# Performance work log

Measured on AMD Instinct MI355X. Metric: run time of the kernel, lower is better.

## Reference

```python
import jax, jax.numpy as jnp
import numpy as np

P, N, NF = 4, 871, 512            # num_meta_paths, node_size (hardcoded 871 in source), node_feature_size
XDIM = 116 * 116                   # x_proj input dim, hardcoded Linear(116*116, nf)
BETA, LAMBDA_WL, GAMMA = 0.1, 0.1, 0.1


def _xavier(k, shape):
    fan_in, fan_out = shape[0], shape[-1]
    bound = np.sqrt(6.0 / (fan_in + fan_out))
    return jax.random.uniform(k, shape, jnp.float32, -bound, bound)


def setup_inputs() -> dict:
    key = jax.random.key(0)
    ks = jax.random.split(key, 12)
    return {
        "z_stack": jax.random.normal(ks[0], (P, N, NF), jnp.float32),
        "x_orig": jax.random.normal(ks[1], (1, 116, 116), jnp.float32),
        "W": _xavier(ks[2], (N, 1)),
        "b": jax.random.uniform(ks[3], (N, 1), jnp.float32),
        "q": _xavier(ks[4], (N, NF)),
        "xp_w": _xavier(ks[5], (XDIM, NF)),
        "xp_b": jnp.zeros((NF,), jnp.float32),
        "w1": _xavier(ks[6], (2 * NF, 512)), "b1": jnp.zeros((512,), jnp.float32),
        "w2": _xavier(ks[7], (512, 256)), "b2": jnp.zeros((256,), jnp.float32),
        "w3": _xavier(ks[8], (256, 1)), "b3": jnp.zeros((1,), jnp.float32),
        "perm": jax.random.permutation(ks[9], N).astype(jnp.int32),
    }


def _mi_mlp(t, w1, b1, w2, b2, w3, b3):
    h = jax.nn.relu(t @ w1 + b1)
    h = jax.nn.relu(h @ w2 + b2)
    return h @ w3 + b3  # [N, 1]


def reference(z_stack, x_orig, W, b, q, xp_w, xp_b, w1, b1, w2, b2, w3, b3, perm):
    # --- vectorized form of the per-node loop:
    # score_p = mean_i( tanh(W_i * z[p,i,:] + b_i) . q_i )
    zt = jnp.tanh(W[None] * z_stack + b[None])            # [P,N,NF]
    scores = jnp.mean(jnp.sum(zt * q[None], axis=-1), axis=-1)  # [P]
    proportions = scores / jnp.sum(scores)
    attn = jax.nn.softmax(proportions)                    # [P] (no isomorphic pairs -> no overwrite)
    # layer_out_p = attn_p * z_p + z_p ; emb = sum_p layer_out_p
    emb = jnp.einsum('p,pnf->nf', 1.0 + attn, z_stack)    # [N,NF]
    # --- estimate_MI(x_orig, emb, mi_estimator_xz)
    x = jnp.broadcast_to(x_orig.reshape(1, -1), (N, XDIM))
    xh = x @ xp_w + xp_b                                  # [N,NF]
    t0 = jnp.concatenate([xh, emb], axis=1)               # [N,2NF]
    t1 = jnp.concatenate([xh, emb[perm]], axis=1)
    mi_lb = jnp.mean(_mi_mlp(t0, w1, b1, w2, b2, w3, b3)) - jnp.log(
        jnp.mean(jnp.exp(_mi_mlp(t1, w1, b1, w2, b2, w3, b3))) + 1e-8)
    I_XZ = jnp.clip(mi_lb, 0.0)
    # y_labels=None -> I_ZY = 0 ; empty isomorphic_pairs -> wl_loss = 0
    total_loss = I_XZ - BETA * 0.0 + LAMBDA_WL * 0.0 + GAMMA * jnp.sum(attn)
    return emb, total_loss
```

## Files before the change

kernel.cpp:

```cpp
#include <hip/hip_runtime.h>
#include <hip/hip_bf16.h>
#include <math.h>

#define NMETA  4
#define NNODE  871
#define NFEAT  512
#define XDIM   (116*116)
#define ZPLANE (NNODE*NFEAT)
#define NCHUNK 55
#define MT     55

#define WS_COEF   8
#define WS_CNT    12
#define WS_SPART  16
#define WS_C1P    256
#define WS_XHP    8448
#define WS_V      73984
#define WS_W1P    74856
#define WS_W2P    205928
#define WS_FXHP   271500
#define WS_FSP    271628
#define MAGICF    0x13579BDFu

typedef short v8s __attribute__((ext_vector_type(8)));
typedef float v4f __attribute__((ext_vector_type(4)));

static __device__ __forceinline__ short f2bf(float f) {
  __hip_bfloat16 h = __float2bfloat16(f);
  return *reinterpret_cast<short*>(&h);
}

__global__ __launch_bounds__(256) void k_front(const float* __restrict__ x,
                                               const float* __restrict__ xpw,
                                               const float* __restrict__ w1,
                                               const float* __restrict__ w2,
                                               const float* __restrict__ z,
                                               const float* __restrict__ W,
                                               const float* __restrict__ b,
                                               const float* __restrict__ q,
                                               const float* __restrict__ xpb,
                                               const float* __restrict__ b1,
                                               float* __restrict__ ws,
                                               short* __restrict__ w1p,
                                               short* __restrict__ w2p) {
  const int blk = blockIdx.x;
  const int tid = threadIdx.x;
  if (blk < 128) {
    const int f4 = tid & 127;
    const int rp = tid >> 7;
    const int d0 = blk * 106;
    const int rows = min(106, XDIM - d0);
    __shared__ float xs[106];
    if (tid < rows) xs[tid] = x[d0 + tid];
    __syncthreads();
    float4 acc = {0.f, 0.f, 0.f, 0.f};
    const float4* xp4 = (const float4*)xpw;
#pragma unroll 4
    for (int r = rp; r < rows; r += 2) {
      const float xv = xs[r];
      const float4 w = xp4[(size_t)(d0 + r) * 128 + f4];
      acc.x += xv * w.x; acc.y += xv * w.y; acc.z += xv * w.z; acc.w += xv * w.w;
    }
    __shared__ float4 red4[128];
    if (rp) red4[f4] = acc;
    __syncthreads();
    if (!rp) {
      float4 o = red4[f4];
      o.x += acc.x; o.y += acc.y; o.z += acc.z; o.w += acc.w;
      ((float4*)(ws + WS_XHP + (size_t)blk * NFEAT))[f4] = o;
    }
    __syncthreads();
    if (tid == 0) {
      __builtin_amdgcn_fence(__ATOMIC_RELEASE, "agent");
      __hip_atomic_store((unsigned*)&ws[WS_FXHP + blk], MAGICF,
                         __ATOMIC_RELAXED, __HIP_MEMORY_SCOPE_AGENT);
    }
  } else if (blk < 512) {
    const int base = (blk - 128) * 256 + tid;
#pragma unroll
    for (int it = 0; it < 4; ++it) {
      int s = base + it * 98304;
      if (s < 262144) {
        const int k = s >> 9, n = s & 511;
        const int t = (k >> 5) * 16384 + (n >> 4) * 512 + ((k >> 3) & 3) * 128
                    + (n & 15) * 8 + (k & 7);
        w1p[t] = f2bf(w1[(size_t)(512 + k) * 512 + n]);
      } else {
        const int o = s - 262144;
        const int k = o >> 8, n = o & 255;
        const int t = (k >> 5) * 8192 + (n >> 4) * 512 + ((k >> 3) & 3) * 128
                    + (n & 15) * 8 + (k & 7);
        w2p[t] = f2bf(w2[(size_t)k * 256 + n]);
      }
    }
  } else if (blk < 732) {
    const int sblk = blk - 512;
    const int p = sblk / NCHUNK;
    const int chunk = sblk % NCHUNK;
    const int i0 = chunk * 16;
    const int i1 = min(i0 + 16, NNODE);
    const int f4 = tid & 127;
    const int ip = tid >> 7;
    float local = 0.f;
    for (int i = i0 + ip; i < i1; i += 2) {
      const float wi = W[i];
      const float bi = b[i];
      const float4 zr = ((const float4*)(z + ((size_t)p * NNODE + i) * NFEAT))[f4];
      const float4 qr = ((const float4*)(q + (size_t)i * NFEAT))[f4];
      local += tanhf(wi * zr.x + bi) * qr.x + tanhf(wi * zr.y + bi) * qr.y
             + tanhf(wi * zr.z + bi) * qr.z + tanhf(wi * zr.w + bi) * qr.w;
    }
    __shared__ float red[256];
    red[tid] = local;
    __syncthreads();
    for (int s = 128; s > 0; s >>= 1) {
      if (tid < s) red[tid] += red[tid + s];
      __syncthreads();
    }
    if (tid == 0) {
      ws[WS_SPART + sblk] = red[0];
      __builtin_amdgcn_fence(__ATOMIC_RELEASE, "agent");
      __hip_atomic_store((unsigned*)&ws[WS_FSP + sblk], MAGICF,
                         __ATOMIC_RELAXED, __HIP_MEMORY_SCOPE_AGENT);
    }
  } else if (blk == 732) {
    if (tid == 0) *(unsigned*)&ws[WS_CNT] = 0u;
  } else if (blk < 749) {
    const int bk = blk - 733;
    for (;;) {
      int ok = 1;
      if (tid < 128)
        ok = (__hip_atomic_load((const unsigned*)&ws[WS_FXHP + tid],
                                __ATOMIC_RELAXED, __HIP_MEMORY_SCOPE_AGENT) == MAGICF);
      if (__syncthreads_and(ok)) break;
      __builtin_amdgcn_s_sleep(8);
    }
    __builtin_amdgcn_fence(__ATOMIC_ACQUIRE, "agent");
    __shared__ float xsc[32];
    {
      const int f = tid & 31;
      const int pg = tid >> 5;
      float s = 0.f;
#pragma unroll 4
      for (int p = pg; p < 128; p += 8)
        s += ws[WS_XHP + (size_t)p * NFEAT + bk * 32 + f];
      __shared__ float redc[256];
      redc[tid] = s;
      __syncthreads();
      if (tid < 32) {
        float t2 = 0.f;
#pragma unroll
        for (int g = 0; g < 8; ++g) t2 += redc[g * 32 + tid];
        xsc[tid] = t2 + xpb[bk * 32 + tid];
      }
      __syncthreads();
    }
    const int j4 = tid & 127;
    const int fp = tid >> 7;
    float4 acc = {0.f, 0.f, 0.f, 0.f};
    const float4* w14 = (const float4*)w1;
#pragma unroll
    for (int ff = 0; ff < 16; ++ff) {
      const int f = bk * 32 + fp * 16 + ff;
      const float xv = xsc[fp * 16 + ff];
      const float4 wv = w14[(size_t)f * 128 + j4];
      acc.x += xv * wv.x; acc.y += xv * wv.y; acc.z += xv * wv.z; acc.w += xv * wv.w;
    }
    __shared__ float4 red2[128];
    if (fp) red2[j4] = acc;
    __syncthreads();
    if (!fp) {
      float4 o = acc;
      {
        float4 t = red2[j4];
        o.x += t.x; o.y += t.y; o.z += t.z; o.w += t.w;
      }
      if (bk == 0) {
        o.x += b1[j4 * 4 + 0]; o.y += b1[j4 * 4 + 1];
        o.z += b1[j4 * 4 + 2]; o.w += b1[j4 * 4 + 3];
      }
      ((float4*)(ws + WS_C1P + (size_t)bk * NFEAT))[j4] = o;
    }
  } else {
    for (;;) {
      int ok = 1;
      if (tid < 220)
        ok = (__hip_atomic_load((const unsigned*)&ws[WS_FSP + tid],
                                __ATOMIC_RELAXED, __HIP_MEMORY_SCOPE_AGENT) == MAGICF);
      if (__syncthreads_and(ok)) break;
      __builtin_amdgcn_s_sleep(8);
    }
    __builtin_amdgcn_fence(__ATOMIC_ACQUIRE, "agent");
    __shared__ float sp[220];
    if (tid < 220) sp[tid] = ws[WS_SPART + tid];
    __syncthreads();
    if (tid == 0) {
      float sv[NMETA], sum = 0.f;
#pragma unroll
      for (int p = 0; p < NMETA; ++p) {
        float s = 0.f;
        for (int c = 0; c < NCHUNK; ++c) s += sp[p * NCHUNK + c];
        sv[p] = s / (float)NNODE;
        sum += sv[p];
      }
      float m = -1e30f;
#pragma unroll
      for (int p = 0; p < NMETA; ++p) { sv[p] = sv[p] / sum; m = fmaxf(m, sv[p]); }
      float es = 0.f;
#pragma unroll
      for (int p = 0; p < NMETA; ++p) { sv[p] = expf(sv[p] - m); es += sv[p]; }
#pragma unroll
      for (int p = 0; p < NMETA; ++p) ws[WS_COEF + p] = 1.f + sv[p] / es;
    }
  }
}

__global__ __launch_bounds__(1024) void k_fused(const float* __restrict__ z,
                                                float* __restrict__ ws,
                                                float* __restrict__ out,
                                                const short* __restrict__ w1p,
                                                const short* __restrict__ w2p,
                                                const float* __restrict__ b2,
                                                const float* __restrict__ w3,
                                                const float* __restrict__ b3) {
  __shared__ __align__(16) short embs[8192];
  __shared__ __align__(16) short h2a[8192];
  __shared__ float cs[512];
  __shared__ float rf0[1024], rf1[1024];
  __shared__ float vred[16][17];
  const int tid = threadIdx.x;
  const int r0 = blockIdx.x * 16;

  if (tid < 512) {
    float a0 = 0.f;
#pragma unroll
    for (int k = 0; k < 16; ++k) a0 += ws[WS_C1P + k * 512 + tid];
    cs[tid] = a0;
  }
  const float c0 = ws[WS_COEF + 0], c1c = ws[WS_COEF + 1];
  const float c2 = ws[WS_COEF + 2], c3 = ws[WS_COEF + 3];

  const int oc = tid & 63;
  const int row = tid >> 6;
  const float4* z4 = (const float4*)z;
  float4* out4 = (float4*)out;
  {
    const int gr = r0 + row;
    const int slot = oc * 16 + (row ^ (oc & 15));
    v8s h;
    if (gr < NNODE) {
      const int zi = gr * 128 + oc * 2;
      float4 a0 = z4[zi],               a1 = z4[zi + 1];
      float4 b0 = z4[NNODE*128 + zi],   b1v = z4[NNODE*128 + zi + 1];
      float4 d0 = z4[2*NNODE*128 + zi], d1 = z4[2*NNODE*128 + zi + 1];
      float4 e0 = z4[3*NNODE*128 + zi], e1 = z4[3*NNODE*128 + zi + 1];
      float4 r0v, r1v;
      r0v.x = c0*a0.x + c1c*b0.x + c2*d0.x + c3*e0.x;
      r0v.y = c0*a0.y + c1c*b0.y + c2*d0.y + c3*e0.y;
      r0v.z = c0*a0.z + c1c*b0.z + c2*d0.z + c3*e0.z;
      r0v.w = c0*a0.w + c1c*b0.w + c2*d0.w + c3*e0.w;
      r1v.x = c0*a1.x + c1c*b1v.x + c2*d1.x + c3*e1.x;
      r1v.y = c0*a1.y + c1c*b1v.y + c2*d1.y + c3*e1.y;
      r1v.z = c0*a1.z + c1c*b1v.z + c2*d1.z + c3*e1.z;
      r1v.w = c0*a1.w + c1c*b1v.w + c2*d1.w + c3*e1.w;
      out4[zi] = r0v;
      out4[zi + 1] = r1v;
      h[0] = f2bf(r0v.x); h[1] = f2bf(r0v.y); h[2] = f2bf(r0v.z); h[3] = f2bf(r0v.w);
      h[4] = f2bf(r1v.x); h[5] = f2bf(r1v.y); h[6] = f2bf(r1v.z); h[7] = f2bf(r1v.w);
    } else {
      h = (v8s){0,0,0,0,0,0,0,0};
    }
    *(v8s*)(embs + slot * 8) = h;
  }
  __syncthreads();

  const int lane = tid & 63, w = tid >> 6;
  const int n15 = lane & 15, quad = lane >> 4;
  v4f e[2];
#pragma unroll
  for (int ct = 0; ct < 2; ++ct) e[ct] = (v4f){0.f, 0.f, 0.f, 0.f};
#pragma unroll
  for (int kb = 0; kb < 16; ++kb) {
    const int koct = kb * 4 + quad;
    v8s a = *(const v8s*)(embs + (koct * 16 + (n15 ^ (koct & 15))) * 8);
    const short* B = w1p + kb * 16384 + w * 1024 + quad * 128 + n15 * 8;
#pragma unroll
    for (int ct = 0; ct < 2; ++ct) {
      v8s bb = *(const v8s*)(B + ct * 512);
      e[ct] = __builtin_amdgcn_mfma_f32_16x16x32_bf16(a, bb, e[ct], 0, 0, 0);
    }
  }
#pragma unroll
  for (int ct = 0; ct < 2; ++ct) {
    const int col = w * 32 + ct * 16 + n15;
    const int koct = col >> 3, j = col & 7;
#pragma unroll
    for (int r = 0; r < 4; ++r) {
      const int m = quad * 4 + r;
      h2a[(koct * 16 + (m ^ (koct & 15))) * 8 + j] = f2bf(fmaxf(e[ct][r] + cs[col], 0.f));
    }
  }
  __syncthreads();

  v4f g = (v4f){0.f, 0.f, 0.f, 0.f};
#pragma unroll
  for (int kb = 0; kb < 16; ++kb) {
    const int koct = kb * 4 + quad;
    v8s a = *(const v8s*)(h2a + (koct * 16 + (n15 ^ (koct & 15))) * 8);
    v8s bb = *(const v8s*)(w2p + kb * 8192 + w * 512 + quad * 128 + n15 * 8);
    g = __builtin_amdgcn_mfma_f32_16x16x32_bf16(a, bb, g, 0, 0, 0);
  }
  {
    const int col = w * 16 + n15;
    const float b2v = b2[col], w3v = w3[col];
#pragma unroll
    for (int r = 0; r < 4; ++r) {
      float s = fmaxf(g[r] + b2v, 0.f) * w3v;
      s += __shfl_xor(s, 1);
      s += __shfl_xor(s, 2);
      s += __shfl_xor(s, 4);
      s += __shfl_xor(s, 8);
      if (n15 == 0) vred[quad * 4 + r][w] = s;
    }
  }
  __syncthreads();
  if (tid < 16) {
    float acc = 0.f;
#pragma unroll
    for (int ww = 0; ww < 16; ++ww) acc += vred[tid][ww];
    const int grow = r0 + tid;
    if (grow < NNODE) ws[WS_V + grow] = acc;
  }

  __shared__ unsigned last;
  __syncthreads();
  if (tid == 0) {
    __threadfence();
    unsigned old = atomicAdd((unsigned int*)&ws[WS_CNT], 1u);
    last = (old == MT - 1) ? 1u : 0u;
  }
  __syncthreads();
  if (last) {
    __builtin_amdgcn_fence(__ATOMIC_ACQUIRE, "agent");
    const float bias = b3[0];
    float s0 = 0.f, s1 = 0.f;
    for (int i = tid; i < NNODE; i += 1024) {
      float xv = ws[WS_V + i] + bias;
      s0 += xv;
      s1 += expf(xv);
    }
    rf0[tid] = s0; rf1[tid] = s1;
    __syncthreads();
    for (int s = 512; s > 0; s >>= 1) {
      if (tid < s) { rf0[tid] += rf0[tid + s]; rf1[tid] += rf1[tid + s]; }
      __syncthreads();
    }
    if (tid == 0) {
      float m0 = rf0[0] / (float)NNODE;
      float m1 = rf1[0] / (float)NNODE;
      float mi = m0 - logf(m1 + 1e-8f);
      out[ZPLANE] = fmaxf(mi, 0.f) + 0.1f;
    }
  }
}

extern "C" void kernel_launch(void* const* d_in, const int* in_sizes, int n_in,
                              void* d_out, int out_size, void* d_ws, size_t ws_size,
                              hipStream_t stream) {
  const float* z   = (const float*)d_in[0];
  const float* x   = (const float*)d_in[1];
  const float* W   = (const float*)d_in[2];
  const float* b   = (const float*)d_in[3];
  const float* q   = (const float*)d_in[4];
  const float* xpw = (const float*)d_in[5];
  const float* xpb = (const float*)d_in[6];
  const float* w1  = (const float*)d_in[7];
  const float* b1  = (const float*)d_in[8];
  const float* w2  = (const float*)d_in[9];
  const float* b2  = (const float*)d_in[10];
  const float* w3  = (const float*)d_in[11];
  const float* b3  = (const float*)d_in[12];
  float* out = (float*)d_out;
  float* ws  = (float*)d_ws;

  short* w1p = (short*)(ws + WS_W1P);
  short* w2p = (short*)(ws + WS_W2P);

  k_front<<<750, 256, 0, stream>>>(x, xpw, w1, w2, z, W, b, q, xpb, b1, ws, w1p, w2p);
  k_fused<<<MT, 1024, 0, stream>>>(z, ws, out, w1p, w2p, b2, w3, b3);
}
```

Measured before the change: 136.3 us.

## Merge front and fused kernels into one persistent kernel with flag-based dataflow

Replaces the two-kernel launch with a single 254-block kernel of 1024 threads. The MLP tile blocks compute their own attention score partials from z rows they already hold in registers, then spin on flags for the score, packed-weight and xh-contribution producers instead of waiting at a kernel boundary. The x-projection, c1 and weight-packing roles are re-split across fewer, larger blocks. The goal is to remove the inter-kernel gap and the second read of z, at the cost of relying on all blocks being co-resident, since blocks spin on flags set by other blocks.

```diff
diff --git a/kernel.cpp b/kernel.cpp
--- a/kernel.cpp
+++ b/kernel.cpp
@@ -7,19 +7,22 @@
 #define NFEAT  512
 #define XDIM   (116*116)
 #define ZPLANE (NNODE*NFEAT)
-#define NCHUNK 55
 #define MT     55
 
-#define WS_COEF   8
-#define WS_CNT    12
+#define NXB    175
+#define XROWS  77
+
 #define WS_SPART  16
 #define WS_C1P    256
 #define WS_XHP    8448
-#define WS_V      73984
-#define WS_W1P    74856
-#define WS_W2P    205928
-#define WS_FXHP   271500
-#define WS_FSP    271628
+#define WS_V      98304
+#define WS_W1P    99328
+#define WS_W2P    230400
+#define WS_FXHP   263168
+#define WS_FPACK  263344
+#define WS_FC1    263368
+#define WS_FSP    263376
+#define WS_FV     263436
 #define MAGICF    0x13579BDFu
 
 typedef short v8s __attribute__((ext_vector_type(8)));
@@ -30,337 +33,373 @@
   return *reinterpret_cast<short*>(&h);
 }
 
-__global__ __launch_bounds__(256) void k_front(const float* __restrict__ x,
-                                               const float* __restrict__ xpw,
-                                               const float* __restrict__ w1,
-                                               const float* __restrict__ w2,
-                                               const float* __restrict__ z,
-                                               const float* __restrict__ W,
-                                               const float* __restrict__ b,
-                                               const float* __restrict__ q,
-                                               const float* __restrict__ xpb,
-                                               const float* __restrict__ b1,
-                                               float* __restrict__ ws,
-                                               short* __restrict__ w1p,
-                                               short* __restrict__ w2p) {
+static __device__ __forceinline__ unsigned ldflag(const float* ws, int off) {
+  return __hip_atomic_load((const unsigned*)&ws[off], __ATOMIC_RELAXED,
+                           __HIP_MEMORY_SCOPE_AGENT);
+}
+static __device__ __forceinline__ void stflag(float* ws, int off) {
+  __builtin_amdgcn_fence(__ATOMIC_RELEASE, "agent");
+  __hip_atomic_store((unsigned*)&ws[off], MAGICF, __ATOMIC_RELAXED,
+                     __HIP_MEMORY_SCOPE_AGENT);
+}
+
+__global__ __launch_bounds__(1024) void k_all(const float* __restrict__ z,
+                                              const float* __restrict__ x,
+                                              const float* __restrict__ W,
+                                              const float* __restrict__ b,
+                                              const float* __restrict__ q,
+                                              const float* __restrict__ xpw,
+                                              const float* __restrict__ xpb,
+                                              const float* __restrict__ w1,
+                                              const float* __restrict__ b1,
+                                              const float* __restrict__ w2,
+                                              const float* __restrict__ b2,
+                                              const float* __restrict__ w3,
+                                              const float* __restrict__ b3,
+                                              float* __restrict__ ws,
+                                              float* __restrict__ out,
+                                              short* __restrict__ w1p,
+                                              short* __restrict__ w2p) {
+  __shared__ __align__(16) char pool[37376];
   const int blk = blockIdx.x;
   const int tid = threadIdx.x;
-  if (blk < 128) {
+
+  if (blk < MT) {
+    short* embs = (short*)pool;
+    short* h2a  = (short*)(pool + 16384);
+    float* cs   = (float*)(pool + 32768);
+    float* spl  = (float*)(pool + 34816);
+    float* sred = (float*)(pool + 35712);
+    float* cf   = (float*)(pool + 35968);
+    float* vred = (float*)(pool + 36000);
+    float* wred = (float*)(pool + 37088);
+
+    const int r0 = blk * 16;
+    const int oc = tid & 63;
+    const int row = tid >> 6;
+    const int gr = r0 + row;
+    const bool valid = gr < NNODE;
+
+    const float4* z4 = (const float4*)z;
+    const float4* q4 = (const float4*)q;
+    float4 za0, za1, zb0, zb1, zc0, zc1, zd0, zd1, qa, qb;
+    float wi = 0.f, bi = 0.f;
+    const int zi = gr * 128 + oc * 2;
+    if (valid) {
+      za0 = z4[zi];                 za1 = z4[zi + 1];
+      zb0 = z4[NNODE*128 + zi];     zb1 = z4[NNODE*128 + zi + 1];
+      zc0 = z4[2*NNODE*128 + zi];   zc1 = z4[2*NNODE*128 + zi + 1];
+      zd0 = z4[3*NNODE*128 + zi];   zd1 = z4[3*NNODE*128 + zi + 1];
+      qa  = q4[gr * 128 + oc * 2];  qb  = q4[gr * 128 + oc * 2 + 1];
+      wi = W[gr]; bi = b[gr];
+    } else {
+      za0 = za1 = zb0 = zb1 = zc0 = zc1 = zd0 = zd1 = (float4){0,0,0,0};
+      qa = qb = (float4){0,0,0,0};
+    }
+
+    auto dot8 = [&](const float4& u0, const float4& u1) -> float {
+      return tanhf(wi*u0.x + bi)*qa.x + tanhf(wi*u0.y + bi)*qa.y
+           + tanhf(wi*u0.z + bi)*qa.z + tanhf(wi*u0.w + bi)*qa.w
+           + tanhf(wi*u1.x + bi)*qb.x + tanhf(wi*u1.y + bi)*qb.y
+           + tanhf(wi*u1.z + bi)*qb.z + tanhf(wi*u1.w + bi)*qb.w;
+    };
+    float sp0 = valid ? dot8(za0, za1) : 0.f;
+    float sp1 = valid ? dot8(zb0, zb1) : 0.f;
+    float sp2 = valid ? dot8(zc0, zc1) : 0.f;
+    float sp3 = valid ? dot8(zd0, zd1) : 0.f;
+#pragma unroll
+    for (int m = 1; m < 64; m <<= 1) {
+      sp0 += __shfl_xor(sp0, m); sp1 += __shfl_xor(sp1, m);
+      sp2 += __shfl_xor(sp2, m); sp3 += __shfl_xor(sp3, m);
+    }
+    if (oc == 0) {
+      sred[row*4+0] = sp0; sred[row*4+1] = sp1;
+      sred[row*4+2] = sp2; sred[row*4+3] = sp3;
+    }
+    __syncthreads();
+    if (tid < 4) {
+      float s = 0.f;
+#pragma unroll
+      for (int r = 0; r < 16; ++r) s += sred[r*4 + tid];
+      ws[WS_SPART + tid * 55 + blk] = s;
+    }
+    __syncthreads();
+    if (tid == 0) stflag(ws, WS_FSP + blk);
+
+    for (;;) {
+      int ok = 1;
+      if (tid < 55) ok = (ldflag(ws, WS_FSP + tid) == MAGICF);
+      if (__syncthreads_and(ok)) break;
+      __builtin_amdgcn_s_sleep(2);
+    }
+    __builtin_amdgcn_fence(__ATOMIC_ACQUIRE, "agent");
+    if (tid < 220) spl[tid] = ws[WS_SPART + tid];
+    __syncthreads();
+    if (tid == 0) {
+      float sv[NMETA], sum = 0.f;
+#pragma unroll
+      for (int p = 0; p < NMETA; ++p) {
+        float s = 0.f;
+        for (int c = 0; c < MT; ++c) s += spl[p * 55 + c];
+        sv[p] = s / (float)NNODE;
+        sum += sv[p];
+      }
+      float m = -1e30f;
+#pragma unroll
+      for (int p = 0; p < NMETA; ++p) { sv[p] = sv[p] / sum; m = fmaxf(m, sv[p]); }
+      float es = 0.f;
+#pragma unroll
+      for (int p = 0; p < NMETA; ++p) { sv[p] = expf(sv[p] - m); es += sv[p]; }
+#pragma unroll
+      for (int p = 0; p < NMETA; ++p) cf[p] = 1.f + sv[p] / es;
+    }
+    __syncthreads();
+    const float c0 = cf[0], c1c = cf[1], c2 = cf[2], c3 = cf[3];
+
+    {
+      const int slot = oc * 16 + (row ^ (oc & 15));
+      v8s h;
+      if (valid) {
+        float4 r0v, r1v;
+        r0v.x = c0*za0.x + c1c*zb0.x + c2*zc0.x + c3*zd0.x;
+        r0v.y = c0*za0.y + c1c*zb0.y + c2*zc0.y + c3*zd0.y;
+        r0v.z = c0*za0.z + c1c*zb0.z + c2*zc0.z + c3*zd0.z;
+        r0v.w = c0*za0.w + c1c*zb0.w + c2*zc0.w + c3*zd0.w;
+        r1v.x = c0*za1.x + c1c*zb1.x + c2*zc1.x + c3*zd1.x;
+        r1v.y = c0*za1.y + c1c*zb1.y + c2*zc1.y + c3*zd1.y;
+        r1v.z = c0*za1.z + c1c*zb1.z + c2*zc1.z + c3*zd1.z;
+        r1v.w = c0*za1.w + c1c*zb1.w + c2*zc1.w + c3*zd1.w;
+        ((float4*)out)[zi] = r0v;
+        ((float4*)out)[zi + 1] = r1v;
+        h[0] = f2bf(r0v.x); h[1] = f2bf(r0v.y); h[2] = f2bf(r0v.z); h[3] = f2bf(r0v.w);
+        h[4] = f2bf(r1v.x); h[5] = f2bf(r1v.y); h[6] = f2bf(r1v.z); h[7] = f2bf(r1v.w);
+      } else {
+        h = (v8s){0,0,0,0,0,0,0,0};
+      }
+      *(v8s*)(embs + slot * 8) = h;
+    }
+    __syncthreads();
+
+    for (;;) {
+      int ok = 1;
+      if (tid < 16) ok = (ldflag(ws, WS_FPACK + tid) == MAGICF);
+      else if (tid < 20) ok = (ldflag(ws, WS_FC1 + (tid - 16)) == MAGICF);
+      if (__syncthreads_and(ok)) break;
+      __builtin_amdgcn_s_sleep(2);
+    }
+    __builtin_amdgcn_fence(__ATOMIC_ACQUIRE, "agent");
+    if (tid < 512) {
+      float a = 0.f;
+#pragma unroll
+      for (int k = 0; k < 4; ++k) a += ws[WS_C1P + k * 512 + tid];
+      cs[tid] = a;
+    }
+    __syncthreads();
+
+    const int lane = tid & 63, w = tid >> 6;
+    const int n15 = lane & 15, quad = lane >> 4;
+    v4f e[2];
+#pragma unroll
+    for (int ct = 0; ct < 2; ++ct) e[ct] = (v4f){0.f, 0.f, 0.f, 0.f};
+#pragma unroll
+    for (int kb = 0; kb < 16; ++kb) {
+      const int koct = kb * 4 + quad;
+      v8s a = *(const v8s*)(embs + (koct * 16 + (n15 ^ (koct & 15))) * 8);
+      const short* B = w1p + kb * 16384 + w * 1024 + quad * 128 + n15 * 8;
+#pragma unroll
+      for (int ct = 0; ct < 2; ++ct) {
+        v8s bb = *(const v8s*)(B + ct * 512);
+        e[ct] = __builtin_amdgcn_mfma_f32_16x16x32_bf16(a, bb, e[ct], 0, 0, 0);
+      }
+    }
+#pragma unroll
+    for (int ct = 0; ct < 2; ++ct) {
+      const int col = w * 32 + ct * 16 + n15;
+      const int koct = col >> 3, j = col & 7;
+#pragma unroll
+      for (int r = 0; r < 4; ++r) {
+        const int m = quad * 4 + r;
+        h2a[(koct * 16 + (m ^ (koct & 15))) * 8 + j] = f2bf(fmaxf(e[ct][r] + cs[col], 0.f));
+      }
+    }
+    __syncthreads();
+
+    for (;;) {
+      int ok = 1;
+      if (tid < 4) ok = (ldflag(ws, WS_FPACK + 16 + tid) == MAGICF);
+      if (__syncthreads_and(ok)) break;
+      __builtin_amdgcn_s_sleep(2);
+    }
+    __builtin_amdgcn_fence(__ATOMIC_ACQUIRE, "agent");
+
+    v4f g = (v4f){0.f, 0.f, 0.f, 0.f};
+#pragma unroll
+    for (int kb = 0; kb < 16; ++kb) {
+      const int koct = kb * 4 + quad;
+      v8s a = *(const v8s*)(h2a + (koct * 16 + (n15 ^ (koct & 15))) * 8);
+      v8s bb = *(const v8s*)(w2p + kb * 8192 + w * 512 + quad * 128 + n15 * 8);
+      g = __builtin_amdgcn_mfma_f32_16x16x32_bf16(a, bb, g, 0, 0, 0);
+    }
+    {
+      const int col = w * 16 + n15;
+      const float b2v = b2[col], w3v = w3[col];
+#pragma unroll
+      for (int r = 0; r < 4; ++r) {
+        float s = fmaxf(g[r] + b2v, 0.f) * w3v;
+        s += __shfl_xor(s, 1);
+        s += __shfl_xor(s, 2);
+        s += __shfl_xor(s, 4);
+        s += __shfl_xor(s, 8);
+        if (n15 == 0) vred[(quad * 4 + r) * 17 + w] = s;
+      }
+    }
+    __syncthreads();
+    if (tid < 16) {
+      float acc = 0.f;
+#pragma unroll
+      for (int ww = 0; ww < 16; ++ww) acc += vred[tid * 17 + ww];
+      const int grow = r0 + tid;
+      if (grow < NNODE) ws[WS_V + grow] = acc;
+    }
+    __syncthreads();
+    if (tid == 0) stflag(ws, WS_FV + blk);
+
+    if (blk == 0) {
+      for (;;) {
+        int ok = 1;
+        if (tid < 55) ok = (ldflag(ws, WS_FV + tid) == MAGICF);
+        if (__syncthreads_and(ok)) break;
+        __builtin_amdgcn_s_sleep(2);
+      }
+      __builtin_amdgcn_fence(__ATOMIC_ACQUIRE, "agent");
+      const float bias = b3[0];
+      float s0 = 0.f, s1 = 0.f;
+      if (tid < NNODE) {
+        float xv = ws[WS_V + tid] + bias;
+        s0 = xv; s1 = expf(xv);
+      }
+#pragma unroll
+      for (int m = 1; m < 64; m <<= 1) { s0 += __shfl_xor(s0, m); s1 += __shfl_xor(s1, m); }
+      if (lane == 0) { wred[w * 2] = s0; wred[w * 2 + 1] = s1; }
+      __syncthreads();
+      if (tid == 0) {
+        float t0 = 0.f, t1 = 0.f;
+#pragma unroll
+        for (int ww = 0; ww < 16; ++ww) { t0 += wred[ww * 2]; t1 += wred[ww * 2 + 1]; }
+        float m0 = t0 / (float)NNODE;
+        float m1 = t1 / (float)NNODE;
+        float mi = m0 - logf(m1 + 1e-8f);
+        out[ZPLANE] = fmaxf(mi, 0.f) + 0.1f;
+      }
+    }
+  } else if (blk < MT + NXB) {
+    const int xb = blk - MT;
+    const int d0 = xb * XROWS;
+    const int rows = min(XROWS, XDIM - d0);
+    float* xs = (float*)pool;
+    float4* redx = (float4*)(pool + 320);
+    if (tid < rows) xs[tid] = x[d0 + tid];
+    __syncthreads();
     const int f4 = tid & 127;
     const int rp = tid >> 7;
-    const int d0 = blk * 106;
-    const int rows = min(106, XDIM - d0);
-    __shared__ float xs[106];
-    if (tid < rows) xs[tid] = x[d0 + tid];
-    __syncthreads();
     float4 acc = {0.f, 0.f, 0.f, 0.f};
     const float4* xp4 = (const float4*)xpw;
-#pragma unroll 4
-    for (int r = rp; r < rows; r += 2) {
+    for (int r = rp; r < rows; r += 8) {
       const float xv = xs[r];
-      const float4 w = xp4[(size_t)(d0 + r) * 128 + f4];
-      acc.x += xv * w.x; acc.y += xv * w.y; acc.z += xv * w.z; acc.w += xv * w.w;
-    }
-    __shared__ float4 red4[128];
-    if (rp) red4[f4] = acc;
+      const float4 wv = xp4[(size_t)(d0 + r) * 128 + f4];
+      acc.x += xv * wv.x; acc.y += xv * wv.y; acc.z += xv * wv.z; acc.w += xv * wv.w;
+    }
+    if (rp) redx[(rp - 1) * 128 + f4] = acc;
     __syncthreads();
     if (!rp) {
-      float4 o = red4[f4];
-      o.x += acc.x; o.y += acc.y; o.z += acc.z; o.w += acc.w;
-      ((float4*)(ws + WS_XHP + (size_t)blk * NFEAT))[f4] = o;
-    }
-    __syncthreads();
-    if (tid == 0) {
-      __builtin_amdgcn_fence(__ATOMIC_RELEASE, "agent");
-      __hip_atomic_store((unsigned*)&ws[WS_FXHP + blk], MAGICF,
-                         __ATOMIC_RELAXED, __HIP_MEMORY_SCOPE_AGENT);
-    }
-  } else if (blk < 512) {
-    const int base = (blk - 128) * 256 + tid;
-#pragma unroll
-    for (int it = 0; it < 4; ++it) {
-      int s = base + it * 98304;
-      if (s < 262144) {
+#pragma unroll
+      for (int g = 0; g < 7; ++g) {
+        float4 t = redx[g * 128 + f4];
+        acc.x += t.x; acc.y += t.y; acc.z += t.z; acc.w += t.w;
+      }
+      ((float4*)(ws + WS_XHP + (size_t)xb * 512))[f4] = acc;
+    }
+    __syncthreads();
+    if (tid == 0) stflag(ws, WS_FXHP + xb);
+  } else if (blk < MT + NXB + 4) {
+    const int bk = blk - (MT + NXB);
+    float* xh = (float*)pool;
+    float* redr = (float*)(pool + 512);
+    float4* redg = (float4*)(pool + 4608);
+    for (;;) {
+      int ok = 1;
+      if (tid < NXB) ok = (ldflag(ws, WS_FXHP + tid) == MAGICF);
+      if (__syncthreads_and(ok)) break;
+      __builtin_amdgcn_s_sleep(2);
+    }
+    __builtin_amdgcn_fence(__ATOMIC_ACQUIRE, "agent");
+    const int f = tid & 127;
+    const int part = tid >> 7;
+    {
+      float s = 0.f;
+      for (int p = part; p < NXB; p += 8) s += ws[WS_XHP + (size_t)p * 512 + bk * 128 + f];
+      redr[tid] = s;
+    }
+    __syncthreads();
+    if (tid < 128) {
+      float t = xpb[bk * 128 + tid];
+#pragma unroll
+      for (int g = 0; g < 8; ++g) t += redr[g * 128 + tid];
+      xh[tid] = t;
+    }
+    __syncthreads();
+    const int j4 = tid & 127;
+    const int fg = tid >> 7;
+    float4 acc = {0.f, 0.f, 0.f, 0.f};
+    const float4* w14 = (const float4*)w1;
+#pragma unroll
+    for (int ff = 0; ff < 16; ++ff) {
+      const int fr = bk * 128 + fg * 16 + ff;
+      const float xv = xh[fg * 16 + ff];
+      const float4 wv = w14[(size_t)fr * 128 + j4];
+      acc.x += xv * wv.x; acc.y += xv * wv.y; acc.z += xv * wv.z; acc.w += xv * wv.w;
+    }
+    if (fg) redg[(fg - 1) * 128 + j4] = acc;
+    __syncthreads();
+    if (!fg) {
+#pragma unroll
+      for (int g = 0; g < 7; ++g) {
+        float4 t = redg[g * 128 + j4];
+        acc.x += t.x; acc.y += t.y; acc.z += t.z; acc.w += t.w;
+      }
+      if (bk == 0) {
+        acc.x += b1[j4 * 4 + 0]; acc.y += b1[j4 * 4 + 1];
+        acc.z += b1[j4 * 4 + 2]; acc.w += b1[j4 * 4 + 3];
+      }
+      ((float4*)(ws + WS_C1P + (size_t)bk * 512))[j4] = acc;
+    }
+    __syncthreads();
+    if (tid == 0) stflag(ws, WS_FC1 + bk);
+  } else {
+    const int pb = blk - (MT + NXB + 4);
+    if (pb < 16) {
+      const int s0 = pb * 16384;
+#pragma unroll
+      for (int it = 0; it < 16; ++it) {
+        const int s = s0 + it * 1024 + tid;
         const int k = s >> 9, n = s & 511;
         const int t = (k >> 5) * 16384 + (n >> 4) * 512 + ((k >> 3) & 3) * 128
                     + (n & 15) * 8 + (k & 7);
         w1p[t] = f2bf(w1[(size_t)(512 + k) * 512 + n]);
-      } else {
-        const int o = s - 262144;
+      }
+    } else {
+      const int o0 = (pb - 16) * 16384;
+#pragma unroll
+      for (int it = 0; it < 16; ++it) {
+        const int o = o0 + it * 1024 + tid;
         const int k = o >> 8, n = o & 255;
         const int t = (k >> 5) * 8192 + (n >> 4) * 512 + ((k >> 3) & 3) * 128
                     + (n & 15) * 8 + (k & 7);
         w2p[t] = f2bf(w2[(size_t)k * 256 + n]);
       }
     }
-  } else if (blk < 732) {
-    const int sblk = blk - 512;
-    const int p = sblk / NCHUNK;
-    const int chunk = sblk % NCHUNK;
-    const int i0 = chunk * 16;
-    const int i1 = min(i0 + 16, NNODE);
-    const int f4 = tid & 127;
-    const int ip = tid >> 7;
-    float local = 0.f;
-    for (int i = i0 + ip; i < i1; i += 2) {
-      const float wi = W[i];
-      const float bi = b[i];
-      const float4 zr = ((const float4*)(z + ((size_t)p * NNODE + i) * NFEAT))[f4];
-      const float4 qr = ((const float4*)(q + (size_t)i * NFEAT))[f4];
-      local += tanhf(wi * zr.x + bi) * qr.x + tanhf(wi * zr.y + bi) * qr.y
-             + tanhf(wi * zr.z + bi) * qr.z + tanhf(wi * zr.w + bi) * qr.w;
-    }
-    __shared__ float red[256];
-    red[tid] = local;
-    __syncthreads();
-    for (int s = 128; s > 0; s >>= 1) {
-      if (tid < s) red[tid] += red[tid + s];
-      __syncthreads();
-    }
-    if (tid == 0) {
-      ws[WS_SPART + sblk] = red[0];
-      __builtin_amdgcn_fence(__ATOMIC_RELEASE, "agent");
-      __hip_atomic_store((unsigned*)&ws[WS_FSP + sblk], MAGICF,
-                         __ATOMIC_RELAXED, __HIP_MEMORY_SCOPE_AGENT);
-    }
-  } else if (blk == 732) {
-    if (tid == 0) *(unsigned*)&ws[WS_CNT] = 0u;
-  } else if (blk < 749) {
-    const int bk = blk - 733;
-    for (;;) {
-      int ok = 1;
-      if (tid < 128)
-        ok = (__hip_atomic_load((const unsigned*)&ws[WS_FXHP + tid],
-                                __ATOMIC_RELAXED, __HIP_MEMORY_SCOPE_AGENT) == MAGICF);
-      if (__syncthreads_and(ok)) break;
-      __builtin_amdgcn_s_sleep(8);
-    }
-    __builtin_amdgcn_fence(__ATOMIC_ACQUIRE, "agent");
-    __shared__ float xsc[32];
-    {
-      const int f = tid & 31;
-      const int pg = tid >> 5;
-      float s = 0.f;
-#pragma unroll 4
-      for (int p = pg; p < 128; p += 8)
-        s += ws[WS_XHP + (size_t)p * NFEAT + bk * 32 + f];
-      __shared__ float redc[256];
-      redc[tid] = s;
-      __syncthreads();
-      if (tid < 32) {
-        float t2 = 0.f;
-#pragma unroll
-        for (int g = 0; g < 8; ++g) t2 += redc[g * 32 + tid];
-        xsc[tid] = t2 + xpb[bk * 32 + tid];
-      }
-      __syncthreads();
-    }
-    const int j4 = tid & 127;
-    const int fp = tid >> 7;
-    float4 acc = {0.f, 0.f, 0.f, 0.f};
-    const float4* w14 = (const float4*)w1;
-#pragma unroll
-    for (int ff = 0; ff < 16; ++ff) {
-      const int f = bk * 32 + fp * 16 + ff;
-      const float xv = xsc[fp * 16 + ff];
-      const float4 wv = w14[(size_t)f * 128 + j4];
-      acc.x += xv * wv.x; acc.y += xv * wv.y; acc.z += xv * wv.z; acc.w += xv * wv.w;
-    }
-    __shared__ float4 red2[128];
-    if (fp) red2[j4] = acc;
-    __syncthreads();
-    if (!fp) {
-      float4 o = acc;
-      {
-        float4 t = red2[j4];
-        o.x += t.x; o.y += t.y; o.z += t.z; o.w += t.w;
-      }
-      if (bk == 0) {
-        o.x += b1[j4 * 4 + 0]; o.y += b1[j4 * 4 + 1];
-        o.z += b1[j4 * 4 + 2]; o.w += b1[j4 * 4 + 3];
-      }
-      ((float4*)(ws + WS_C1P + (size_t)bk * NFEAT))[j4] = o;
-    }
-  } else {
-    for (;;) {
-      int ok = 1;
-      if (tid < 220)
-        ok = (__hip_atomic_load((const unsigned*)&ws[WS_FSP + tid],
-                                __ATOMIC_RELAXED, __HIP_MEMORY_SCOPE_AGENT) == MAGICF);
-      if (__syncthreads_and(ok)) break;
-      __builtin_amdgcn_s_sleep(8);
-    }
-    __builtin_amdgcn_fence(__ATOMIC_ACQUIRE, "agent");
-    __shared__ float sp[220];
-    if (tid < 220) sp[tid] = ws[WS_SPART + tid];
-    __syncthreads();
-    if (tid == 0) {
-      float sv[NMETA], sum = 0.f;
-#pragma unroll
-      for (int p = 0; p < NMETA; ++p) {
-        float s = 0.f;
-        for (int c = 0; c < NCHUNK; ++c) s += sp[p * NCHUNK + c];
-        sv[p] = s / (float)NNODE;
-        sum += sv[p];
-      }
-      float m = -1e30f;
-#pragma unroll
-      for (int p = 0; p < NMETA; ++p) { sv[p] = sv[p] / sum; m = fmaxf(m, sv[p]); }
-      float es = 0.f;
-#pragma unroll
-      for (int p = 0; p < NMETA; ++p) { sv[p] = expf(sv[p] - m); es += sv[p]; }
-#pragma unroll
-      for (int p = 0; p < NMETA; ++p) ws[WS_COEF + p] = 1.f + sv[p] / es;
-    }
-  }
-}
-
-__global__ __launch_bounds__(1024) void k_fused(const float* __restrict__ z,
-                                                float* __restrict__ ws,
-                                                float* __restrict__ out,
-                                                const short* __restrict__ w1p,
-                                                const short* __restrict__ w2p,
-                                                const float* __restrict__ b2,
-                                                const float* __restrict__ w3,
-                                                const float* __restrict__ b3) {
-  __shared__ __align__(16) short embs[8192];
-  __shared__ __align__(16) short h2a[8192];
-  __shared__ float cs[512];
-  __shared__ float rf0[1024], rf1[1024];
-  __shared__ float vred[16][17];
-  const int tid = threadIdx.x;
-  const int r0 = blockIdx.x * 16;
-
-  if (tid < 512) {
-    float a0 = 0.f;
-#pragma unroll
-    for (int k = 0; k < 16; ++k) a0 += ws[WS_C1P + k * 512 + tid];
-    cs[tid] = a0;
-  }
-  const float c0 = ws[WS_COEF + 0], c1c = ws[WS_COEF + 1];
-  const float c2 = ws[WS_COEF + 2], c3 = ws[WS_COEF + 3];
-
-  const int oc = tid & 63;
-  const int row = tid >> 6;
-  const float4* z4 = (const float4*)z;
-  float4* out4 = (float4*)out;
-  {
-    const int gr = r0 + row;
-    const int slot = oc * 16 + (row ^ (oc & 15));
-    v8s h;
-    if (gr < NNODE) {
-      const int zi = gr * 128 + oc * 2;
-      float4 a0 = z4[zi],               a1 = z4[zi + 1];
-      float4 b0 = z4[NNODE*128 + zi],   b1v = z4[NNODE*128 + zi + 1];
-      float4 d0 = z4[2*NNODE*128 + zi], d1 = z4[2*NNODE*128 + zi + 1];
-      float4 e0 = z4[3*NNODE*128 + zi], e1 = z4[3*NNODE*128 + zi + 1];
-      float4 r0v, r1v;
-      r0v.x = c0*a0.x + c1c*b0.x + c2*d0.x + c3*e0.x;
-      r0v.y = c0*a0.y + c1c*b0.y + c2*d0.y + c3*e0.y;
-      r0v.z = c0*a0.z + c1c*b0.z + c2*d0.z + c3*e0.z;
-      r0v.w = c0*a0.w + c1c*b0.w + c2*d0.w + c3*e0.w;
-      r1v.x = c0*a1.x + c1c*b1v.x + c2*d1.x + c3*e1.x;
-      r1v.y = c0*a1.y + c1c*b1v.y + c2*d1.y + c3*e1.y;
-      r1v.z = c0*a1.z + c1c*b1v.z + c2*d1.z + c3*e1.z;
-      r1v.w = c0*a1.w + c1c*b1v.w + c2*d1.w + c3*e1.w;
-      out4[zi] = r0v;
-      out4[zi + 1] = r1v;
-      h[0] = f2bf(r0v.x); h[1] = f2bf(r0v.y); h[2] = f2bf(r0v.z); h[3] = f2bf(r0v.w);
-      h[4] = f2bf(r1v.x); h[5] = f2bf(r1v.y); h[6] = f2bf(r1v.z); h[7] = f2bf(r1v.w);
-    } else {
-      h = (v8s){0,0,0,0,0,0,0,0};
-    }
-    *(v8s*)(embs + slot * 8) = h;
-  }
-  __syncthreads();
-
-  const int lane = tid & 63, w = tid >> 6;
-  const int n15 = lane & 15, quad = lane >> 4;
-  v4f e[2];
-#pragma unroll
-  for (int ct = 0; ct < 2; ++ct) e[ct] = (v4f){0.f, 0.f, 0.f, 0.f};
-#pragma unroll
-  for (int kb = 0; kb < 16; ++kb) {
-    const int koct = kb * 4 + quad;
-    v8s a = *(const v8s*)(embs + (koct * 16 + (n15 ^ (koct & 15))) * 8);
-    const short* B = w1p + kb * 16384 + w * 1024 + quad * 128 + n15 * 8;
-#pragma unroll
-    for (int ct = 0; ct < 2; ++ct) {
-      v8s bb = *(const v8s*)(B + ct * 512);
-      e[ct] = __builtin_amdgcn_mfma_f32_16x16x32_bf16(a, bb, e[ct], 0, 0, 0);
-    }
-  }
-#pragma unroll
-  for (int ct = 0; ct < 2; ++ct) {
-    const int col = w * 32 + ct * 16 + n15;
-    const int koct = col >> 3, j = col & 7;
-#pragma unroll
-    for (int r = 0; r < 4; ++r) {
-      const int m = quad * 4 + r;
-      h2a[(koct * 16 + (m ^ (koct & 15))) * 8 + j] = f2bf(fmaxf(e[ct][r] + cs[col], 0.f));
-    }
-  }
-  __syncthreads();
-
-  v4f g = (v4f){0.f, 0.f, 0.f, 0.f};
-#pragma unroll
-  for (int kb = 0; kb < 16; ++kb) {
-    const int koct = kb * 4 + quad;
-    v8s a = *(const v8s*)(h2a + (koct * 16 + (n15 ^ (koct & 15))) * 8);
-    v8s bb = *(const v8s*)(w2p + kb * 8192 + w * 512 + quad * 128 + n15 * 8);
-    g = __builtin_amdgcn_mfma_f32_16x16x32_bf16(a, bb, g, 0, 0, 0);
-  }
-  {
-    const int col = w * 16 + n15;
-    const float b2v = b2[col], w3v = w3[col];
-#pragma unroll
-    for (int r = 0; r < 4; ++r) {
-      float s = fmaxf(g[r] + b2v, 0.f) * w3v;
-      s += __shfl_xor(s, 1);
-      s += __shfl_xor(s, 2);
-      s += __shfl_xor(s, 4);
-      s += __shfl_xor(s, 8);
-      if (n15 == 0) vred[quad * 4 + r][w] = s;
-    }
-  }
-  __syncthreads();
-  if (tid < 16) {
-    float acc = 0.f;
-#pragma unroll
-    for (int ww = 0; ww < 16; ++ww) acc += vred[tid][ww];
-    const int grow = r0 + tid;
-    if (grow < NNODE) ws[WS_V + grow] = acc;
-  }
-
-  __shared__ unsigned last;
-  __syncthreads();
-  if (tid == 0) {
-    __threadfence();
-    unsigned old = atomicAdd((unsigned int*)&ws[WS_CNT], 1u);
-    last = (old == MT - 1) ? 1u : 0u;
-  }
-  __syncthreads();
-  if (last) {
-    __builtin_amdgcn_fence(__ATOMIC_ACQUIRE, "agent");
-    const float bias = b3[0];
-    float s0 = 0.f, s1 = 0.f;
-    for (int i = tid; i < NNODE; i += 1024) {
-      float xv = ws[WS_V + i] + bias;
-      s0 += xv;
-      s1 += expf(xv);
-    }
-    rf0[tid] = s0; rf1[tid] = s1;
-    __syncthreads();
-    for (int s = 512; s > 0; s >>= 1) {
-      if (tid < s) { rf0[tid] += rf0[tid + s]; rf1[tid] += rf1[tid + s]; }
-      __syncthreads();
-    }
-    if (tid == 0) {
-      float m0 = rf0[0] / (float)NNODE;
-      float m1 = rf1[0] / (float)NNODE;
-      float mi = m0 - logf(m1 + 1e-8f);
-      out[ZPLANE] = fmaxf(mi, 0.f) + 0.1f;
-    }
+    __syncthreads();
+    if (tid == 0) stflag(ws, WS_FPACK + pb);
   }
 }
 
@@ -386,6 +425,6 @@
   short* w1p = (short*)(ws + WS_W1P);
   short* w2p = (short*)(ws + WS_W2P);
 
-  k_front<<<750, 256, 0, stream>>>(x, xpw, w1, w2, z, W, b, q, xpb, b1, ws, w1p, w2p);
-  k_fused<<<MT, 1024, 0, stream>>>(z, ws, out, w1p, w2p, b2, w3, b3);
+  k_all<<<MT + NXB + 4 + 20, 1024, 0, stream>>>(z, x, W, b, q, xpw, xpb, w1, b1,
+                                                w2, b2, w3, b3, ws, out, w1p, w2p);
 }
```

New measurement: 152.1 us. 11.5% more time.
